# Optimization experiments

Hardware: AMD Instinct MI355X
Metric: run time of the kernel (lower is better)

The kernel has to match this reference:

```python
import jax, jax.numpy as jnp
import numpy as np

B, D, H = 131072, 256, 4
NUM_EXPERTS = 4


def setup_inputs() -> dict:
    key = jax.random.key(0)
    ks = jax.random.split(key, 32)
    s = 0.02
    w = lambda k, shape: (jax.random.normal(k, shape, jnp.float32) * s)
    z = lambda shape: jnp.zeros(shape, jnp.float32)
    return {
        "z_gat": jax.random.normal(ks[0], (B, D), jnp.float32),
        "z_gin": jax.random.normal(ks[1], (B, D), jnp.float32),
        # gate: Linear(2D -> 4)
        "gate_W": w(ks[2], (2 * D, NUM_EXPERTS)), "gate_b": z((NUM_EXPERTS,)),
        # expert 0: ConcatFusion  fc1(2D->D), fc2(D->D)
        "c_W1": w(ks[3], (2 * D, D)), "c_b1": z((D,)),
        "c_W2": w(ks[4], (D, D)), "c_b2": z((D,)),
        # expert 1: MulFusion fc1(D->D), fc2(D->D)
        "m_W1": w(ks[5], (D, D)), "m_b1": z((D,)),
        "m_W2": w(ks[6], (D, D)), "m_b2": z((D,)),
        # expert 2: CrossAttnFusion (MHA in/out proj + fc)
        "a_Wq": w(ks[7], (D, D)), "a_bq": z((D,)),
        "a_Wk": w(ks[8], (D, D)), "a_bk": z((D,)),
        "a_Wv": w(ks[9], (D, D)), "a_bv": z((D,)),
        "a_Wo": w(ks[10], (D, D)), "a_bo": z((D,)),
        "a_Wfc": w(ks[11], (D, D)), "a_bfc": z((D,)),
        # expert 3: WeightedSumFusion fc_alpha(2D->D), fc_out(D->D)
        "w_Wa": w(ks[12], (2 * D, D)), "w_ba": z((D,)),
        "w_Wo": w(ks[13], (D, D)), "w_bo": z((D,)),
    }


def reference(z_gat, z_gin, gate_W, gate_b,
              c_W1, c_b1, c_W2, c_b2,
              m_W1, m_b1, m_W2, m_b2,
              a_Wq, a_bq, a_Wk, a_bk, a_Wv, a_bv, a_Wo, a_bo, a_Wfc, a_bfc,
              w_Wa, w_ba, w_Wo, w_bo):
    x = jnp.concatenate([z_gat, z_gin], axis=-1)          # (B, 2D)
    gate_probs = jax.nn.softmax(x @ gate_W + gate_b, -1)  # (B, 4)
    topk_p, topk_i = jax.lax.top_k(gate_probs, 1)         # k = 1
    probs = topk_p[:, 0]
    idx = topk_i[:, 0]

    def concat_expert():
        h = jax.nn.relu(x @ c_W1 + c_b1)
        return h @ c_W2 + c_b2

    def mul_expert():
        h = jax.nn.relu((z_gat * z_gin) @ m_W1 + m_b1)
        return h @ m_W2 + m_b2

    def attn_expert():
        zs = jnp.stack([z_gat, z_gin], axis=1)            # (B, 2, D)
        hd = D // H
        q = (zs @ a_Wq + a_bq).reshape(-1, 2, H, hd)
        k = (zs @ a_Wk + a_bk).reshape(-1, 2, H, hd)
        v = (zs @ a_Wv + a_bv).reshape(-1, 2, H, hd)
        scale = 1.0 / float(np.sqrt(hd))
        sc = jnp.einsum('bqhd,bkhd->bhqk', q, k) * scale  # (B, H, 2, 2)
        a = jax.nn.softmax(sc, -1)
        o = jnp.einsum('bhqk,bkhd->bqhd', a, v).reshape(-1, 2, D)
        o = o @ a_Wo + a_bo                               # (B, 2, D)
        return o.mean(axis=1) @ a_Wfc + a_bfc

    def wsum_expert():
        alpha = jax.nn.sigmoid(x @ w_Wa + w_ba)
        h = alpha * z_gat + (1.0 - alpha) * z_gin
        return h @ w_Wo + w_bo

    expert_outs = [concat_expert(), mul_expert(), attn_expert(), wsum_expert()]

    output = jnp.zeros_like(z_gat)
    counts = []
    for e in range(NUM_EXPERTS):
        sel = idx == e                                    # disjoint masks since k=1
        cnt = sel.sum()
        # original: scalar mean of selected gate probs, weighting whole expert output
        avg = jnp.where(cnt > 0,
                        jnp.sum(probs * sel) / jnp.maximum(cnt, 1).astype(probs.dtype),
                        jnp.asarray(0.0, probs.dtype))
        output = output + jnp.where(sel[:, None], avg * expert_outs[e], 0.0)
        counts.append(cnt)

    usage = jnp.stack(counts).astype(jnp.float32) / B
    aux_loss = jnp.sum(usage ** 2) * float(NUM_EXPERTS)
    # dropout is identity in eval mode
    return output, aux_loss
```

## Files before the change

kernel.cpp:

```cpp
#include <hip/hip_runtime.h>
#include <math.h>

#define BN 131072
#define DD 256
#define NE 4

typedef unsigned short u16;
typedef __bf16 bf16x8 __attribute__((ext_vector_type(8)));
typedef float f32x4 __attribute__((ext_vector_type(4)));

__device__ __forceinline__ u16 f2bf(float f) {
  union { float f; unsigned int u; } v; v.f = f;
  unsigned int u = v.u;
  unsigned int r = (u + 0x7FFFu + ((u >> 16) & 1u)) >> 16;
  return (u16)r;
}
__device__ __forceinline__ float bf2f(u16 x) {
  union { unsigned int u; float f; } v; v.u = ((unsigned int)x) << 16; return v.f;
}

#define WS_SWZ_OFF 2097216
#define BCOMB_OFF  3670080

#define OFF_CW1  0
#define OFF_CW2  131072
#define OFF_MW1  196608
#define OFF_MW2  262144
#define OFF_AWQ  327680
#define OFF_AWK  393216
#define OFF_AWV  458752
#define OFF_WCB  524288
#define OFF_WWA  589824
#define OFF_WWO  720896
#define SWZ_TOTAL_GROUPS 98304

#define G_ATTN   768
#define G_CONCAT 768
#define G_MUL    768
#define G_WSUM   768
#define G_TOTAL  3072

__global__ void k_init(int* __restrict__ listpos, double* __restrict__ psum) {
  int t = threadIdx.x;
  if (t < NE) { listpos[t] = 0; psum[t] = 0.0; }
}

__global__ __launch_bounds__(256) void k_wcomb(
    const float* __restrict__ Wo, const float* __restrict__ bo,
    const float* __restrict__ Wfc, const float* __restrict__ bfc,
    float* __restrict__ Wc, float* __restrict__ bc) {
  int n = threadIdx.x;
  int k = blockIdx.x;
  if (k < 256) {
    float acc = 0.f;
    #pragma unroll 8
    for (int j = 0; j < 256; ++j) acc += Wo[k * 256 + j] * Wfc[j * 256 + n];
    Wc[k * 256 + n] = acc;
  } else {
    float acc = bfc[n];
    #pragma unroll 8
    for (int j = 0; j < 256; ++j) acc += bo[j] * Wfc[j * 256 + n];
    bc[n] = acc;
  }
}

struct SwzArgs {
  const float* src[10];
  int KS[10];
  int lks[10];
  int dstoff[10];
  int gbase[10];
};

__global__ __launch_bounds__(256) void k_swz(SwzArgs a, u16* __restrict__ dst) {
  int g = blockIdx.x * 256 + threadIdx.x;
  if (g >= SWZ_TOTAL_GROUPS) return;
  int i = 0;
  #pragma unroll
  for (int t = 1; t < 10; ++t) if (g >= a.gbase[t]) i = t;
  int gl = g - a.gbase[i];
  int KS = a.KS[i], lks = a.lks[i];
  int l = gl & 63, t2 = gl >> 6;
  int ks = t2 & (KS - 1), ct = t2 >> lks;
  const float* src = a.src[i] + (size_t)(ks * 32 + ((l >> 4) << 3)) * 256 + ct * 16 + (l & 15);
  u16 tmp[8];
  #pragma unroll
  for (int j = 0; j < 8; ++j) tmp[j] = f2bf(src[(size_t)j * 256]);
  uint4 pk;
  pk.x = (unsigned)tmp[0] | ((unsigned)tmp[1] << 16);
  pk.y = (unsigned)tmp[2] | ((unsigned)tmp[3] << 16);
  pk.z = (unsigned)tmp[4] | ((unsigned)tmp[5] << 16);
  pk.w = (unsigned)tmp[6] | ((unsigned)tmp[7] << 16);
  *(uint4*)(dst + a.dstoff[i] + (size_t)gl * 8) = pk;
}

__global__ __launch_bounds__(256) void k_gate(
    const float* __restrict__ zg, const float* __restrict__ zn,
    const float* __restrict__ gW, const float* __restrict__ gb,
    int* __restrict__ listpos, double* __restrict__ psum,
    int* __restrict__ lists) {
  __shared__ float xs[32 * 129];
  __shared__ double gwd[512 * 4];
  __shared__ double xr[128 * 4];
  __shared__ int    wcnt[4][4];
  __shared__ double wps[4][4];
  __shared__ int    wbase[4][4];
  int tid = threadIdx.x, lane = tid & 63, wave = tid >> 6;
  int rlocal = tid & 127, khalf = tid >> 7;
  int rowbase = blockIdx.x * 128;
  for (int i = tid; i < 2048; i += 256) gwd[i] = (double)gW[i];
  double l0, l1, l2, l3;
  if (khalf) { l0 = l1 = l2 = l3 = 0.0; }
  else { l0 = (double)gb[0]; l1 = (double)gb[1]; l2 = (double)gb[2]; l3 = (double)gb[3]; }

  float4 pf[4];
  #pragma unroll
  for (int j = 0; j < 4; ++j) {
    int idx = tid + j * 256;
    int row = idx >> 3, off = idx & 7;
    pf[j] = *(const float4*)(zg + (size_t)(rowbase + row) * DD + off * 4);
  }

  for (int c = 0; c < 16; ++c) {
    __syncthreads();
    #pragma unroll
    for (int j = 0; j < 4; ++j) {
      int idx = tid + j * 256;
      int row = idx >> 3, off = idx & 7;
      float4 v = pf[j];
      xs[(off * 4 + 0) * 129 + row] = v.x;
      xs[(off * 4 + 1) * 129 + row] = v.y;
      xs[(off * 4 + 2) * 129 + row] = v.z;
      xs[(off * 4 + 3) * 129 + row] = v.w;
    }
    if (c < 15) {
      const float* src = (c + 1 < 8) ? zg : zn;
      int ko = ((c + 1) & 7) * 32;
      #pragma unroll
      for (int j = 0; j < 4; ++j) {
        int idx = tid + j * 256;
        int row = idx >> 3, off = idx & 7;
        pf[j] = *(const float4*)(src + (size_t)(rowbase + row) * DD + ko + off * 4);
      }
    }
    __syncthreads();
    const double* gp = gwd + (size_t)(c * 32 + khalf * 16) * 4;
    int xbase = (khalf * 16) * 129 + rlocal;
    #pragma unroll
    for (int i = 0; i < 16; ++i) {
      double x = (double)xs[xbase + i * 129];
      l0 = fma(x, gp[i * 4 + 0], l0);
      l1 = fma(x, gp[i * 4 + 1], l1);
      l2 = fma(x, gp[i * 4 + 2], l2);
      l3 = fma(x, gp[i * 4 + 3], l3);
    }
  }

  __syncthreads();
  if (khalf) {
    xr[rlocal * 4 + 0] = l0; xr[rlocal * 4 + 1] = l1;
    xr[rlocal * 4 + 2] = l2; xr[rlocal * 4 + 3] = l3;
  }
  __syncthreads();
  int e = -1;
  double p = 0.0;
  if (!khalf) {
    l0 += xr[rlocal * 4 + 0]; l1 += xr[rlocal * 4 + 1];
    l2 += xr[rlocal * 4 + 2]; l3 += xr[rlocal * 4 + 3];
    e = 0; double lm = l0;
    if (l1 > lm) { lm = l1; e = 1; }
    if (l2 > lm) { lm = l2; e = 2; }
    if (l3 > lm) { lm = l3; e = 3; }
    double s = exp(l0 - lm) + exp(l1 - lm) + exp(l2 - lm) + exp(l3 - lm);
    p = 1.0 / s;
  }
  int row = rowbase + rlocal;

  unsigned long long msk[4];
  int cnt[4];
  double pvs[4];
  #pragma unroll
  for (int ee = 0; ee < NE; ++ee) {
    bool mine = (e == ee);
    msk[ee] = __ballot(mine);
    cnt[ee] = __popcll(msk[ee]);
    double pv = mine ? p : 0.0;
    #pragma unroll
    for (int off = 32; off; off >>= 1) pv += __shfl_down(pv, off);
    pvs[ee] = pv;
  }
  if (lane == 0) {
    #pragma unroll
    for (int ee = 0; ee < NE; ++ee) { wcnt[wave][ee] = cnt[ee]; wps[wave][ee] = pvs[ee]; }
  }
  __syncthreads();
  if (tid < NE) {
    int ee = tid;
    int c0 = wcnt[0][ee], c1 = wcnt[1][ee], c2 = wcnt[2][ee], c3 = wcnt[3][ee];
    int tot = c0 + c1 + c2 + c3;
    int base = 0;
    if (tot) {
      base = atomicAdd(&listpos[ee], tot);
      atomicAdd(&psum[ee], wps[0][ee] + wps[1][ee] + wps[2][ee] + wps[3][ee]);
    }
    wbase[0][ee] = base;
    wbase[1][ee] = base + c0;
    wbase[2][ee] = base + c0 + c1;
    wbase[3][ee] = base + c0 + c1 + c2;
  }
  __syncthreads();
  #pragma unroll
  for (int ee = 0; ee < NE; ++ee) {
    if (e == ee) {
      int rank = __popcll(msk[ee] & ((1ull << lane) - 1ull));
      lists[(size_t)ee * BN + wbase[wave][ee] + rank] = row;
    }
  }
}

__global__ void k_finalize(const int* __restrict__ listpos,
                           const double* __restrict__ psum,
                           float* __restrict__ avg, float* __restrict__ aux_out) {
  if (threadIdx.x == 0) {
    double aux = 0.0;
    for (int ee = 0; ee < NE; ++ee) {
      int c = listpos[ee];
      avg[ee] = (c > 0) ? (float)(psum[ee] / (double)c) : 0.0f;
      double u = (double)c / (double)BN;
      aux += u * u;
    }
    *aux_out = (float)(aux * (double)NE);
  }
}

template <int KS, int RB>
__device__ __forceinline__ void mfma_gemm_p(const u16* __restrict__ A, int strideA,
                                            const u16* __restrict__ W,
                                            int wave, int lane, f32x4 acc[RB][4]) {
  int q = lane >> 4, m = lane & 15;
  const u16* wb = W + (((size_t)(wave * 4 * KS) * 64 + lane) << 3);
  bf16x8 b0[4], b1[4];
  #pragma unroll
  for (int i = 0; i < 4; ++i)
    b0[i] = *(const bf16x8*)(wb + (((size_t)(i * KS) * 64) << 3));
  #pragma unroll 1
  for (int ks = 0; ks < KS; ks += 2) {
    #pragma unroll
    for (int i = 0; i < 4; ++i)
      b1[i] = *(const bf16x8*)(wb + (((size_t)(i * KS + ks + 1) * 64) << 3));
    bf16x8 a[RB];
    #pragma unroll
    for (int rb = 0; rb < RB; ++rb)
      a[rb] = *(const bf16x8*)(A + (rb * 16 + m) * strideA + ks * 32 + (q << 3));
    #pragma unroll
    for (int i = 0; i < 4; ++i)
      #pragma unroll
      for (int rb = 0; rb < RB; ++rb)
        acc[rb][i] = __builtin_amdgcn_mfma_f32_16x16x32_bf16(a[rb], b0[i], acc[rb][i], 0, 0, 0);
    if (ks + 2 < KS) {
      #pragma unroll
      for (int i = 0; i < 4; ++i)
        b0[i] = *(const bf16x8*)(wb + (((size_t)(i * KS + ks + 2) * 64) << 3));
    }
    #pragma unroll
    for (int rb = 0; rb < RB; ++rb)
      a[rb] = *(const bf16x8*)(A + (rb * 16 + m) * strideA + (ks + 1) * 32 + (q << 3));
    #pragma unroll
    for (int i = 0; i < 4; ++i)
      #pragma unroll
      for (int rb = 0; rb < RB; ++rb)
        acc[rb][i] = __builtin_amdgcn_mfma_f32_16x16x32_bf16(a[rb], b1[i], acc[rb][i], 0, 0, 0);
  }
}

struct ExpArgs {
  const float* zg; const float* zn;
  const u16* CW1; const u16* CW2; const float* cb1; const float* cb2;
  const u16* MW1; const u16* MW2; const float* mb1; const float* mb2;
  const u16* AWQ; const u16* AWK; const u16* AWV;
  const float* abq; const float* abk; const float* abv;
  const u16* WCB; const float* bcomb;
  const u16* WWA; const u16* WWO; const float* wba; const float* wbo;
  const int* listpos; const int* lists; const float* avgp;
  float* out;
};

__global__ __launch_bounds__(256) void k_experts(ExpArgs A) {
  __shared__ __align__(16) u16 smem[25088];
  __shared__ int rl[32];
  int tid = threadIdx.x, lane = tid & 63, wave = tid >> 6;
  int q = lane >> 4, m = lane & 15;
  int bid = blockIdx.x;

  if (bid < G_ATTN) {
    int bidl = bid;
    int n = A.listpos[2];
    const int* lst = A.lists + 2 * (size_t)BN;
    float scale = A.avgp[2];
    u16* X  = smem;
    u16* Mb = smem + 8448;
    float bqv[4], bkv[4], bvv[4];
    #pragma unroll
    for (int i = 0; i < 4; ++i) {
      int c = wave * 64 + i * 16 + m;
      bqv[i] = A.abq[c]; bkv[i] = A.abk[c]; bvv[i] = A.abv[c];
    }
    for (int tile = bidl; tile * 16 < n; tile += G_ATTN) {
      int base = tile * 16;
      __syncthreads();
      if (tid < 16) rl[tid] = (base + tid < n) ? lst[base + tid] : -1;
      __syncthreads();
      #pragma unroll
      for (int j = 0; j < 8; ++j) {
        int t = tid + j * 256;
        int v = t >> 6, off = t & 63;
        int r = rl[v >> 1];
        float4 val = make_float4(0.f, 0.f, 0.f, 0.f);
        if (r >= 0)
          val = (v & 1) ? *(const float4*)(A.zn + (size_t)r * DD + off * 4)
                        : *(const float4*)(A.zg + (size_t)r * DD + off * 4);
        ushort4 pk; pk.x = f2bf(val.x); pk.y = f2bf(val.y); pk.z = f2bf(val.z); pk.w = f2bf(val.w);
        *(ushort4*)(X + v * 264 + off * 4) = pk;
      }
      __syncthreads();
      f32x4 qa[2][4] = {};
      mfma_gemm_p<8, 2>(X, 264, A.AWQ, wave, lane, qa);
      #pragma unroll
      for (int rb = 0; rb < 2; ++rb)
        #pragma unroll
        for (int i = 0; i < 4; ++i)
          #pragma unroll
          for (int r = 0; r < 4; ++r) qa[rb][i][r] += bqv[i];
      f32x4 ka[2][4] = {};
      mfma_gemm_p<8, 2>(X, 264, A.AWK, wave, lane, ka);
      #pragma unroll
      for (int rb = 0; rb < 2; ++rb)
        #pragma unroll
        for (int i = 0; i < 4; ++i)
          #pragma unroll
          for (int r = 0; r < 4; ++r) ka[rb][i][r] += bkv[i];
      float C0[2][2], C1[2][2];
      #pragma unroll
      for (int rb = 0; rb < 2; ++rb) {
        #pragma unroll
        for (int pr = 0; pr < 2; ++pr) {
          float p00 = 0.f, p01 = 0.f, p10 = 0.f, p11 = 0.f;
          #pragma unroll
          for (int i = 0; i < 4; ++i) {
            float q0 = qa[rb][i][2 * pr], q1 = qa[rb][i][2 * pr + 1];
            float ke = ka[rb][i][2 * pr], ko = ka[rb][i][2 * pr + 1];
            p00 += q0 * ke; p01 += q0 * ko;
            p10 += q1 * ke; p11 += q1 * ko;
          }
          #pragma unroll
          for (int msk = 1; msk < 16; msk <<= 1) {
            p00 += __shfl_xor(p00, msk);
            p01 += __shfl_xor(p01, msk);
            p10 += __shfl_xor(p10, msk);
            p11 += __shfl_xor(p11, msk);
          }
          float s00 = 1.f / (1.f + __expf((p01 - p00) * 0.125f));
          float s10 = 1.f / (1.f + __expf((p11 - p10) * 0.125f));
          float c0 = 0.5f * (s00 + s10);
          C0[rb][pr] = c0; C1[rb][pr] = 1.f - c0;
        }
      }
      f32x4 va[2][4] = {};
      mfma_gemm_p<8, 2>(X, 264, A.AWV, wave, lane, va);
      #pragma unroll
      for (int rb = 0; rb < 2; ++rb)
        #pragma unroll
        for (int pr = 0; pr < 2; ++pr) {
          int rloc = rb * 8 + q * 2 + pr;
          #pragma unroll
          for (int i = 0; i < 4; ++i) {
            float mv = C0[rb][pr] * va[rb][i][2 * pr]
                     + C1[rb][pr] * va[rb][i][2 * pr + 1] + bvv[i];
            Mb[rloc * 264 + wave * 64 + i * 16 + m] = f2bf(mv);
          }
        }
      __syncthreads();
      f32x4 ac[1][4] = {};
      mfma_gemm_p<8, 1>(Mb, 264, A.WCB, wave, lane, ac);
      #pragma unroll
      for (int i = 0; i < 4; ++i) {
        int c = (wave * 4 + i) * 16 + m;
        float bb = A.bcomb[c];
        #pragma unroll
        for (int r = 0; r < 4; ++r) {
          int row = rl[q * 4 + r];
          if (row >= 0) A.out[(size_t)row * DD + c] = (ac[0][i][r] + bb) * scale;
        }
      }
    }
  } else if (bid < G_ATTN + G_CONCAT) {
    int bidl = bid - G_ATTN;
    int n = A.listpos[0];
    const int* lst = A.lists + 0 * (size_t)BN;
    float scale = A.avgp[0];
    u16* X = smem;
    u16* H = smem + 16640;
    for (int tile = bidl; tile * 32 < n; tile += G_CONCAT) {
      int base = tile * 32;
      __syncthreads();
      if (tid < 32) rl[tid] = (base + tid < n) ? lst[base + tid] : -1;
      __syncthreads();
      #pragma unroll
      for (int j = 0; j < 16; ++j) {
        int t = tid + j * 256;
        int row = t >> 7, off = t & 127;
        int r = rl[row];
        float4 v = make_float4(0.f, 0.f, 0.f, 0.f);
        if (r >= 0)
          v = (off < 64) ? *(const float4*)(A.zg + (size_t)r * DD + off * 4)
                         : *(const float4*)(A.zn + (size_t)r * DD + (off - 64) * 4);
        ushort4 pk; pk.x = f2bf(v.x); pk.y = f2bf(v.y); pk.z = f2bf(v.z); pk.w = f2bf(v.w);
        *(ushort4*)(X + row * 520 + off * 4) = pk;
      }
      __syncthreads();
      f32x4 acc[2][4] = {};
      mfma_gemm_p<16, 2>(X, 520, A.CW1, wave, lane, acc);
      #pragma unroll
      for (int i = 0; i < 4; ++i) {
        int c = (wave * 4 + i) * 16 + m;
        float bb = A.cb1[c];
        #pragma unroll
        for (int rb = 0; rb < 2; ++rb)
          #pragma unroll
          for (int r = 0; r < 4; ++r)
            H[(rb * 16 + q * 4 + r) * 264 + c] = f2bf(fmaxf(acc[rb][i][r] + bb, 0.f));
      }
      __syncthreads();
      f32x4 acc2[2][4] = {};
      mfma_gemm_p<8, 2>(H, 264, A.CW2, wave, lane, acc2);
      #pragma unroll
      for (int i = 0; i < 4; ++i) {
        int c = (wave * 4 + i) * 16 + m;
        float bb = A.cb2[c];
        #pragma unroll
        for (int rb = 0; rb < 2; ++rb)
          #pragma unroll
          for (int r = 0; r < 4; ++r) {
            int row = rl[rb * 16 + q * 4 + r];
            if (row >= 0) A.out[(size_t)row * DD + c] = (acc2[rb][i][r] + bb) * scale;
          }
      }
    }
  } else if (bid < G_ATTN + G_CONCAT + G_MUL) {
    int bidl = bid - (G_ATTN + G_CONCAT);
    int n = A.listpos[1];
    const int* lst = A.lists + 1 * (size_t)BN;
    float scale = A.avgp[1];
    u16* X = smem;
    u16* H = smem + 8448;
    for (int tile = bidl; tile * 32 < n; tile += G_MUL) {
      int base = tile * 32;
      __syncthreads();
      if (tid < 32) rl[tid] = (base + tid < n) ? lst[base + tid] : -1;
      __syncthreads();
      #pragma unroll
      for (int j = 0; j < 8; ++j) {
        int t = tid + j * 256;
        int row = t >> 6, off = t & 63;
        int r = rl[row];
        float4 v = make_float4(0.f, 0.f, 0.f, 0.f);
        if (r >= 0) {
          float4 g = *(const float4*)(A.zg + (size_t)r * DD + off * 4);
          float4 h = *(const float4*)(A.zn + (size_t)r * DD + off * 4);
          v = make_float4(g.x * h.x, g.y * h.y, g.z * h.z, g.w * h.w);
        }
        ushort4 pk; pk.x = f2bf(v.x); pk.y = f2bf(v.y); pk.z = f2bf(v.z); pk.w = f2bf(v.w);
        *(ushort4*)(X + row * 264 + off * 4) = pk;
      }
      __syncthreads();
      f32x4 acc[2][4] = {};
      mfma_gemm_p<8, 2>(X, 264, A.MW1, wave, lane, acc);
      #pragma unroll
      for (int i = 0; i < 4; ++i) {
        int c = (wave * 4 + i) * 16 + m;
        float bb = A.mb1[c];
        #pragma unroll
        for (int rb = 0; rb < 2; ++rb)
          #pragma unroll
          for (int r = 0; r < 4; ++r)
            H[(rb * 16 + q * 4 + r) * 264 + c] = f2bf(fmaxf(acc[rb][i][r] + bb, 0.f));
      }
      __syncthreads();
      f32x4 acc2[2][4] = {};
      mfma_gemm_p<8, 2>(H, 264, A.MW2, wave, lane, acc2);
      #pragma unroll
      for (int i = 0; i < 4; ++i) {
        int c = (wave * 4 + i) * 16 + m;
        float bb = A.mb2[c];
        #pragma unroll
        for (int rb = 0; rb < 2; ++rb)
          #pragma unroll
          for (int r = 0; r < 4; ++r) {
            int row = rl[rb * 16 + q * 4 + r];
            if (row >= 0) A.out[(size_t)row * DD + c] = (acc2[rb][i][r] + bb) * scale;
          }
      }
    }
  } else {
    int bidl = bid - (G_ATTN + G_CONCAT + G_MUL);
    int n = A.listpos[3];
    const int* lst = A.lists + 3 * (size_t)BN;
    float scale = A.avgp[3];
    u16* X = smem;
    u16* H = smem + 16640;
    for (int tile = bidl; tile * 32 < n; tile += G_WSUM) {
      int base = tile * 32;
      __syncthreads();
      if (tid < 32) rl[tid] = (base + tid < n) ? lst[base + tid] : -1;
      __syncthreads();
      #pragma unroll
      for (int j = 0; j < 16; ++j) {
        int t = tid + j * 256;
        int row = t >> 7, off = t & 127;
        int r = rl[row];
        float4 v = make_float4(0.f, 0.f, 0.f, 0.f);
        if (r >= 0)
          v = (off < 64) ? *(const float4*)(A.zg + (size_t)r * DD + off * 4)
                         : *(const float4*)(A.zn + (size_t)r * DD + (off - 64) * 4);
        ushort4 pk; pk.x = f2bf(v.x); pk.y = f2bf(v.y); pk.z = f2bf(v.z); pk.w = f2bf(v.w);
        *(ushort4*)(X + row * 520 + off * 4) = pk;
      }
      __syncthreads();
      f32x4 acc[2][4] = {};
      mfma_gemm_p<16, 2>(X, 520, A.WWA, wave, lane, acc);
      #pragma unroll
      for (int i = 0; i < 4; ++i) {
        int c = (wave * 4 + i) * 16 + m;
        float bb = A.wba[c];
        #pragma unroll
        for (int rb = 0; rb < 2; ++rb)
          #pragma unroll
          for (int r = 0; r < 4; ++r) {
            int vr = rb * 16 + q * 4 + r;
            float al = 1.f / (1.f + __expf(-(acc[rb][i][r] + bb)));
            float xg = bf2f(X[vr * 520 + c]);
            float xn = bf2f(X[vr * 520 + 256 + c]);
            H[vr * 264 + c] = f2bf(al * xg + (1.f - al) * xn);
          }
      }
      __syncthreads();
      f32x4 acc2[2][4] = {};
      mfma_gemm_p<8, 2>(H, 264, A.WWO, wave, lane, acc2);
      #pragma unroll
      for (int i = 0; i < 4; ++i) {
        int c = (wave * 4 + i) * 16 + m;
        float bb = A.wbo[c];
        #pragma unroll
        for (int rb = 0; rb < 2; ++rb)
          #pragma unroll
          for (int r = 0; r < 4; ++r) {
            int row = rl[rb * 16 + q * 4 + r];
            if (row >= 0) A.out[(size_t)row * DD + c] = (acc2[rb][i][r] + bb) * scale;
          }
      }
    }
  }
}

extern "C" void kernel_launch(void* const* d_in, const int* in_sizes, int n_in,
                              void* d_out, int out_size, void* d_ws, size_t ws_size,
                              hipStream_t stream) {
  const float* zg   = (const float*)d_in[0];
  const float* zn   = (const float*)d_in[1];
  const float* gW   = (const float*)d_in[2];
  const float* gb   = (const float*)d_in[3];
  const float* cW1  = (const float*)d_in[4];
  const float* cb1  = (const float*)d_in[5];
  const float* cW2  = (const float*)d_in[6];
  const float* cb2  = (const float*)d_in[7];
  const float* mW1  = (const float*)d_in[8];
  const float* mb1  = (const float*)d_in[9];
  const float* mW2  = (const float*)d_in[10];
  const float* mb2  = (const float*)d_in[11];
  const float* aWq  = (const float*)d_in[12];
  const float* abq  = (const float*)d_in[13];
  const float* aWk  = (const float*)d_in[14];
  const float* abk  = (const float*)d_in[15];
  const float* aWv  = (const float*)d_in[16];
  const float* abv  = (const float*)d_in[17];
  const float* aWo  = (const float*)d_in[18];
  const float* abo  = (const float*)d_in[19];
  const float* aWfc = (const float*)d_in[20];
  const float* abfc = (const float*)d_in[21];
  const float* wWa  = (const float*)d_in[22];
  const float* wba  = (const float*)d_in[23];
  const float* wWo  = (const float*)d_in[24];
  const float* wbo  = (const float*)d_in[25];
  float* out = (float*)d_out;

  char* ws = (char*)d_ws;
  double* psum  = (double*)ws;
  int* listpos  = (int*)(ws + 32);
  float* avg    = (float*)(ws + 48);
  int* lists    = (int*)(ws + 64);
  u16* wsw      = (u16*)(ws + WS_SWZ_OFF);
  float* wcf32  = (float*)(ws + 64);
  float* bcomb  = (float*)(ws + BCOMB_OFF);

  SwzArgs sa;
  const float* srcs[10] = {cW1, cW2, mW1, mW2, aWq, aWk, aWv, wcf32, wWa, wWo};
  const int   kss[10]  = {16, 8, 8, 8, 8, 8, 8, 8, 16, 8};
  const int   offs[10] = {OFF_CW1, OFF_CW2, OFF_MW1, OFF_MW2, OFF_AWQ, OFF_AWK,
                          OFF_AWV, OFF_WCB, OFF_WWA, OFF_WWO};
  int gb_acc = 0;
  for (int i = 0; i < 10; ++i) {
    sa.src[i] = srcs[i];
    sa.KS[i] = kss[i];
    sa.lks[i] = (kss[i] == 16) ? 4 : 3;
    sa.dstoff[i] = offs[i];
    sa.gbase[i] = gb_acc;
    gb_acc += kss[i] * 1024;
  }

  ExpArgs ea;
  ea.zg = zg; ea.zn = zn;
  ea.CW1 = wsw + OFF_CW1; ea.CW2 = wsw + OFF_CW2; ea.cb1 = cb1; ea.cb2 = cb2;
  ea.MW1 = wsw + OFF_MW1; ea.MW2 = wsw + OFF_MW2; ea.mb1 = mb1; ea.mb2 = mb2;
  ea.AWQ = wsw + OFF_AWQ; ea.AWK = wsw + OFF_AWK; ea.AWV = wsw + OFF_AWV;
  ea.abq = abq; ea.abk = abk; ea.abv = abv;
  ea.WCB = wsw + OFF_WCB; ea.bcomb = bcomb;
  ea.WWA = wsw + OFF_WWA; ea.WWO = wsw + OFF_WWO; ea.wba = wba; ea.wbo = wbo;
  ea.listpos = listpos; ea.lists = lists; ea.avgp = avg;
  ea.out = out;

  hipLaunchKernelGGL(k_init, dim3(1), dim3(64), 0, stream, listpos, psum);
  hipLaunchKernelGGL(k_wcomb, dim3(257), dim3(256), 0, stream,
                     aWo, abo, aWfc, abfc, wcf32, bcomb);
  hipLaunchKernelGGL(k_swz, dim3(SWZ_TOTAL_GROUPS / 256), dim3(256), 0, stream, sa, wsw);
  hipLaunchKernelGGL(k_gate, dim3(BN / 128), dim3(256), 0, stream,
                     zg, zn, gW, gb, listpos, psum, lists);
  hipLaunchKernelGGL(k_finalize, dim3(1), dim3(64), 0, stream,
                     listpos, psum, avg, out + (size_t)BN * DD);
  hipLaunchKernelGGL(k_experts, dim3(G_TOTAL), dim3(256), 0, stream, ea);
}
```

Measured before the change: 614.3 us.

## Interleave expert blocks by weighted groups, stage swizzle via LDS, deepen gate prefetch

Expert blocks are now interleaved in groups of 48 with a 22/10/6/10 split (attention/concat/mul/wsum), replacing the contiguous equal split. This gives the heavier attention expert more blocks and mixes expert types across CUs. The weight swizzle kernel now loads 32x256 fp32 tiles coalesced into shared memory before writing the bf16 swizzled layout. The gate kernel prefetches two chunks ahead instead of one. The new split is tuned to the expected expert mix, and the gate kernel keeps some unused leftover variables.

```diff
diff --git a/kernel.cpp b/kernel.cpp
--- a/kernel.cpp
+++ b/kernel.cpp
@@ -32,12 +32,15 @@
 #define OFF_WCB  524288
 #define OFF_WWA  589824
 #define OFF_WWO  720896
-#define SWZ_TOTAL_GROUPS 98304
-
-#define G_ATTN   768
-#define G_CONCAT 768
-#define G_MUL    768
-#define G_WSUM   768
+
+#define GRP      48
+#define A_END    22
+#define C_END    32
+#define M_END    38
+#define G_ATTN   (64 * 22)
+#define G_CONCAT (64 * 10)
+#define G_MUL    (64 * 6)
+#define G_WSUM   (64 * 10)
 #define G_TOTAL  3072
 
 __global__ void k_init(int* __restrict__ listpos, double* __restrict__ psum) {
@@ -67,31 +70,45 @@
 struct SwzArgs {
   const float* src[10];
   int KS[10];
-  int lks[10];
   int dstoff[10];
-  int gbase[10];
+  int ksbase[10];
 };
 
 __global__ __launch_bounds__(256) void k_swz(SwzArgs a, u16* __restrict__ dst) {
-  int g = blockIdx.x * 256 + threadIdx.x;
-  if (g >= SWZ_TOTAL_GROUPS) return;
+  __shared__ float ls[32][261];
+  int b = blockIdx.x, tid = threadIdx.x;
   int i = 0;
   #pragma unroll
-  for (int t = 1; t < 10; ++t) if (g >= a.gbase[t]) i = t;
-  int gl = g - a.gbase[i];
-  int KS = a.KS[i], lks = a.lks[i];
-  int l = gl & 63, t2 = gl >> 6;
-  int ks = t2 & (KS - 1), ct = t2 >> lks;
-  const float* src = a.src[i] + (size_t)(ks * 32 + ((l >> 4) << 3)) * 256 + ct * 16 + (l & 15);
-  u16 tmp[8];
+  for (int t = 1; t < 10; ++t) if (b >= a.ksbase[t]) i = t;
+  int ks = b - a.ksbase[i];
+  int KS = a.KS[i];
+  const float* src = a.src[i] + (size_t)ks * 32 * 256;
   #pragma unroll
-  for (int j = 0; j < 8; ++j) tmp[j] = f2bf(src[(size_t)j * 256]);
-  uint4 pk;
-  pk.x = (unsigned)tmp[0] | ((unsigned)tmp[1] << 16);
-  pk.y = (unsigned)tmp[2] | ((unsigned)tmp[3] << 16);
-  pk.z = (unsigned)tmp[4] | ((unsigned)tmp[5] << 16);
-  pk.w = (unsigned)tmp[6] | ((unsigned)tmp[7] << 16);
-  *(uint4*)(dst + a.dstoff[i] + (size_t)gl * 8) = pk;
+  for (int j = 0; j < 8; ++j) {
+    int idx = tid + j * 256;
+    int row = idx >> 6, col4 = idx & 63;
+    float4 v = *(const float4*)(src + (size_t)row * 256 + col4 * 4);
+    ls[row][col4 * 4 + 0] = v.x;
+    ls[row][col4 * 4 + 1] = v.y;
+    ls[row][col4 * 4 + 2] = v.z;
+    ls[row][col4 * 4 + 3] = v.w;
+  }
+  __syncthreads();
+  #pragma unroll
+  for (int t = 0; t < 4; ++t) {
+    int cidx = tid + t * 256;
+    int ct = cidx >> 6, l = cidx & 63;
+    u16 tmp[8];
+    #pragma unroll
+    for (int j = 0; j < 8; ++j)
+      tmp[j] = f2bf(ls[(l >> 4) * 8 + j][ct * 16 + (l & 15)]);
+    uint4 pk;
+    pk.x = (unsigned)tmp[0] | ((unsigned)tmp[1] << 16);
+    pk.y = (unsigned)tmp[2] | ((unsigned)tmp[3] << 16);
+    pk.z = (unsigned)tmp[4] | ((unsigned)tmp[5] << 16);
+    pk.w = (unsigned)tmp[6] | ((unsigned)tmp[7] << 16);
+    *(uint4*)(dst + a.dstoff[i] + (((size_t)(ct * KS + ks) * 64 + l) << 3)) = pk;
+  }
 }
 
 __global__ __launch_bounds__(256) void k_gate(
@@ -113,12 +130,17 @@
   if (khalf) { l0 = l1 = l2 = l3 = 0.0; }
   else { l0 = (double)gb[0]; l1 = (double)gb[1]; l2 = (double)gb[2]; l3 = (double)gb[3]; }
 
-  float4 pf[4];
+  int prow = tid >> 3, poff = tid & 7;
+  const float* rowp = zg + (size_t)(rowbase + prow) * DD;
+  const float* rown = zn + (size_t)(rowbase + prow) * DD;
+
+  float4 pfA[4], pfB[4];
   #pragma unroll
   for (int j = 0; j < 4; ++j) {
     int idx = tid + j * 256;
     int row = idx >> 3, off = idx & 7;
-    pf[j] = *(const float4*)(zg + (size_t)(rowbase + row) * DD + off * 4);
+    pfA[j] = *(const float4*)(zg + (size_t)(rowbase + row) * DD + off * 4);
+    pfB[j] = *(const float4*)(zg + (size_t)(rowbase + row) * DD + 32 + off * 4);
   }
 
   for (int c = 0; c < 16; ++c) {
@@ -127,20 +149,22 @@
     for (int j = 0; j < 4; ++j) {
       int idx = tid + j * 256;
       int row = idx >> 3, off = idx & 7;
-      float4 v = pf[j];
+      float4 v = pfA[j];
       xs[(off * 4 + 0) * 129 + row] = v.x;
       xs[(off * 4 + 1) * 129 + row] = v.y;
       xs[(off * 4 + 2) * 129 + row] = v.z;
       xs[(off * 4 + 3) * 129 + row] = v.w;
     }
-    if (c < 15) {
-      const float* src = (c + 1 < 8) ? zg : zn;
-      int ko = ((c + 1) & 7) * 32;
+    #pragma unroll
+    for (int j = 0; j < 4; ++j) pfA[j] = pfB[j];
+    if (c + 2 < 16) {
+      const float* src = (c + 2 < 8) ? zg : zn;
+      int ko = ((c + 2) & 7) * 32;
       #pragma unroll
       for (int j = 0; j < 4; ++j) {
         int idx = tid + j * 256;
         int row = idx >> 3, off = idx & 7;
-        pf[j] = *(const float4*)(src + (size_t)(rowbase + row) * DD + ko + off * 4);
+        pfB[j] = *(const float4*)(src + (size_t)(rowbase + row) * DD + ko + off * 4);
       }
     }
     __syncthreads();
@@ -155,6 +179,7 @@
       l3 = fma(x, gp[i * 4 + 3], l3);
     }
   }
+  (void)rowp; (void)rown; (void)poff;
 
   __syncthreads();
   if (khalf) {
@@ -290,10 +315,10 @@
   __shared__ int rl[32];
   int tid = threadIdx.x, lane = tid & 63, wave = tid >> 6;
   int q = lane >> 4, m = lane & 15;
-  int bid = blockIdx.x;
-
-  if (bid < G_ATTN) {
-    int bidl = bid;
+  int grp = blockIdx.x / GRP, sub = blockIdx.x % GRP;
+
+  if (sub < A_END) {
+    int bidl = grp * 22 + sub;
     int n = A.listpos[2];
     const int* lst = A.lists + 2 * (size_t)BN;
     float scale = A.avgp[2];
@@ -393,8 +418,8 @@
         }
       }
     }
-  } else if (bid < G_ATTN + G_CONCAT) {
-    int bidl = bid - G_ATTN;
+  } else if (sub < C_END) {
+    int bidl = grp * 10 + (sub - A_END);
     int n = A.listpos[0];
     const int* lst = A.lists + 0 * (size_t)BN;
     float scale = A.avgp[0];
@@ -446,8 +471,8 @@
           }
       }
     }
-  } else if (bid < G_ATTN + G_CONCAT + G_MUL) {
-    int bidl = bid - (G_ATTN + G_CONCAT);
+  } else if (sub < M_END) {
+    int bidl = grp * 6 + (sub - C_END);
     int n = A.listpos[1];
     const int* lst = A.lists + 1 * (size_t)BN;
     float scale = A.avgp[1];
@@ -502,7 +527,7 @@
       }
     }
   } else {
-    int bidl = bid - (G_ATTN + G_CONCAT + G_MUL);
+    int bidl = grp * 10 + (sub - M_END);
     int n = A.listpos[3];
     const int* lst = A.lists + 3 * (size_t)BN;
     float scale = A.avgp[3];
@@ -607,14 +632,13 @@
   const int   kss[10]  = {16, 8, 8, 8, 8, 8, 8, 8, 16, 8};
   const int   offs[10] = {OFF_CW1, OFF_CW2, OFF_MW1, OFF_MW2, OFF_AWQ, OFF_AWK,
                           OFF_AWV, OFF_WCB, OFF_WWA, OFF_WWO};
-  int gb_acc = 0;
+  int ks_acc = 0;
   for (int i = 0; i < 10; ++i) {
     sa.src[i] = srcs[i];
     sa.KS[i] = kss[i];
-    sa.lks[i] = (kss[i] == 16) ? 4 : 3;
     sa.dstoff[i] = offs[i];
-    sa.gbase[i] = gb_acc;
-    gb_acc += kss[i] * 1024;
+    sa.ksbase[i] = ks_acc;
+    ks_acc += kss[i];
   }
 
   ExpArgs ea;
@@ -631,7 +655,7 @@
   hipLaunchKernelGGL(k_init, dim3(1), dim3(64), 0, stream, listpos, psum);
   hipLaunchKernelGGL(k_wcomb, dim3(257), dim3(256), 0, stream,
                      aWo, abo, aWfc, abfc, wcf32, bcomb);
-  hipLaunchKernelGGL(k_swz, dim3(SWZ_TOTAL_GROUPS / 256), dim3(256), 0, stream, sa, wsw);
+  hipLaunchKernelGGL(k_swz, dim3(96), dim3(256), 0, stream, sa, wsw);
   hipLaunchKernelGGL(k_gate, dim3(BN / 128), dim3(256), 0, stream,
                      zg, zn, gW, gb, listpos, psum, lists);
   hipLaunchKernelGGL(k_finalize, dim3(1), dim3(64), 0, stream,
```

Result: no change. 605.5 us (-1.4%).
